# Optimization experiments

Measured on AMD Instinct MI355X. Metric: run time of the kernel, lower is better.

The kernel has to match this reference:

```python
import jax, jax.numpy as jnp
import numpy as np

B, N, C, NPOINT, NSAMPLE, NHEAD, NLAYERS, DOUT = 8, 4096, 128, 1024, 32, 4, 2, 256
EPS = 1e-5


def setup_inputs() -> dict:
    key = jax.random.key(0)
    ks = jax.random.split(key, 12)
    rn = lambda k, s: jax.random.normal(k, s, jnp.float32) * 0.05
    return {
        "xyz": jax.random.normal(ks[0], (B, 3, N), jnp.float32),
        "features": jax.random.normal(ks[1], (B, C, N), jnp.float32),
        # position-encoding MLP (1x1 convs) + BatchNorm2d (inference, running mean=0 var=1)
        "pe_w1": rn(ks[2], (C // 2, 3)), "pe_b1": jnp.zeros((C // 2,), jnp.float32),
        "bn_g": jnp.ones((C // 2,), jnp.float32), "bn_b": jnp.zeros((C // 2,), jnp.float32),
        "pe_w2": rn(ks[3], (C, C // 2)), "pe_b2": jnp.zeros((C,), jnp.float32),
        # 2 pre-norm transformer encoder layers (stacked params)
        "in_w": rn(ks[4], (NLAYERS, 3 * C, C)), "in_b": jnp.zeros((NLAYERS, 3 * C), jnp.float32),
        "out_w": rn(ks[5], (NLAYERS, C, C)), "out_b": jnp.zeros((NLAYERS, C), jnp.float32),
        "ln1_g": jnp.ones((NLAYERS, C), jnp.float32), "ln1_b": jnp.zeros((NLAYERS, C), jnp.float32),
        "ln2_g": jnp.ones((NLAYERS, C), jnp.float32), "ln2_b": jnp.zeros((NLAYERS, C), jnp.float32),
        "ff1_w": rn(ks[6], (NLAYERS, 2 * C, C)), "ff1_b": jnp.zeros((NLAYERS, 2 * C), jnp.float32),
        "ff2_w": rn(ks[7], (NLAYERS, C, 2 * C)), "ff2_b": jnp.zeros((NLAYERS, C), jnp.float32),
        # final 1x1 conv (fc)
        "fc_w": rn(ks[8], (DOUT, C)), "fc_b": jnp.zeros((DOUT,), jnp.float32),
    }


def _fps(pts, npoint):
    # pts: [B, N, 3]; iterative farthest point sampling (start at index 0)
    b, n, _ = pts.shape
    d0 = jnp.full((b, n), 1e10, pts.dtype)
    f0 = jnp.zeros((b,), jnp.int32)

    def step(carry, _):
        dist, far = carry
        c = jnp.take_along_axis(pts, far[:, None, None], axis=1)  # [B,1,3]
        d = jnp.sum((pts - c) ** 2, axis=-1)                      # [B,N]
        dist = jnp.minimum(dist, d)
        return (dist, jnp.argmax(dist, axis=-1).astype(jnp.int32)), far

    _, idx = jax.lax.scan(step, (d0, f0), None, length=npoint)
    return idx.T  # [B, npoint]


def _knn(nsample, pts, queries):
    # pts [B,N,3], queries [B,S,3] -> [B,S,nsample] nearest-neighbor indices
    sqd = (jnp.sum(queries ** 2, -1)[:, :, None] + jnp.sum(pts ** 2, -1)[:, None, :]
           - 2.0 * jnp.einsum('bsc,bnc->bsn', queries, pts))
    _, idx = jax.lax.top_k(-sqd, nsample)
    return idx


_gather = jax.vmap(lambda p, i: p[i])  # per-batch fancy gather


def _ln(x, g, b):
    m = jnp.mean(x, -1, keepdims=True)
    v = jnp.var(x, -1, keepdims=True)
    return (x - m) * jax.lax.rsqrt(v + EPS) * g + b


def _forward(xyz, features, pe_w1, pe_b1, bn_g, bn_b, pe_w2, pe_b2,
             in_w, in_b, out_w, out_b, ln1_g, ln1_b, ln2_g, ln2_b,
             ff1_w, ff1_b, ff2_w, ff2_b, fc_w, fc_b):
    xyz_t = xyz.transpose(0, 2, 1)                      # [B,N,3]
    fps_idx = _fps(xyz_t, NPOINT)                       # [B,S]
    new_xyz = _gather(xyz_t, fps_idx)                   # [B,S,3]
    gidx = _knn(NSAMPLE, xyz_t, new_xyz)                # [B,S,ns]
    gxyz = _gather(xyz_t, gidx)                         # [B,S,ns,3]
    gfeat = _gather(features.transpose(0, 2, 1), gidx)  # [B,S,ns,C]

    # position encoding: 1x1 conv MLP, BN in inference mode (mean=0, var=1)
    h = gxyz @ pe_w1.T + pe_b1
    h = h / jnp.sqrt(jnp.float32(1.0 + EPS)) * bn_g + bn_b
    pe = jax.nn.relu(h) @ pe_w2.T + pe_b2               # [B,S,ns,C]

    x = (gfeat + pe).reshape(B * NPOINT, NSAMPLE, C)    # groups as batch, seq=ns
    hd = C // NHEAD
    scale = 1.0 / jnp.sqrt(jnp.float32(hd))
    for l in range(NLAYERS):
        hN = _ln(x, ln1_g[l], ln1_b[l])
        qkv = hN @ in_w[l].T + in_b[l]
        q, k, v = jnp.split(qkv, 3, axis=-1)
        q = q.reshape(-1, NSAMPLE, NHEAD, hd)
        k = k.reshape(-1, NSAMPLE, NHEAD, hd)
        v = v.reshape(-1, NSAMPLE, NHEAD, hd)
        att = jax.nn.softmax(jnp.einsum('mqhd,mkhd->mhqk', q, k) * scale, axis=-1)
        a = jnp.einsum('mhqk,mkhd->mqhd', att, v).reshape(-1, NSAMPLE, C)
        x = x + (a @ out_w[l].T + out_b[l])
        h2 = _ln(x, ln2_g[l], ln2_b[l])
        x = x + (jax.nn.relu(h2 @ ff1_w[l].T + ff1_b[l]) @ ff2_w[l].T + ff2_b[l])

    pooled = x.reshape(B, NPOINT, NSAMPLE, C).max(axis=2)  # maxpool over neighbors
    out = pooled @ fc_w.T + fc_b                           # [B,S,DOUT]
    return new_xyz.transpose(0, 2, 1), out.transpose(0, 2, 1)


def reference(xyz, features, pe_w1, pe_b1, bn_g, bn_b, pe_w2, pe_b2,
              in_w, in_b, out_w, out_b, ln1_g, ln1_b, ln2_g, ln2_b,
              ff1_w, ff1_b, ff2_w, ff2_b, fc_w, fc_b):
    return _forward(xyz, features, pe_w1, pe_b1, bn_g, bn_b, pe_w2, pe_b2,
                    in_w, in_b, out_w, out_b, ln1_g, ln1_b, ln2_g, ln2_b,
                    ff1_w, ff1_b, ff2_w, ff2_b, fc_w, fc_b)
```

## Files before the change

### kernel.cpp

```cpp
#include <hip/hip_runtime.h>

typedef unsigned int u32;
typedef unsigned long long u64;
typedef unsigned short u16;
typedef __attribute__((ext_vector_type(8))) short bf16x8;
typedef __attribute__((ext_vector_type(4))) float f32x4;

#define DEV __device__ __forceinline__

DEV float sq3(float x, float y, float z) {
#pragma clang fp contract(off)
  return (x * x + y * y) + z * z;
}
DEV float knn_sqd(float4 Q, float4 p) {
#pragma clang fp contract(off)
  float dot = (Q.x * p.x + Q.y * p.y) + Q.z * p.z;
  return (Q.w + p.w) - 2.0f * dot;
}
DEV float dot4(float4 a, float4 b) {
  return (a.x * b.x + a.y * b.y) + (a.z * b.z + a.w * b.w);
}
DEV u32 f2bfu(float f) {
  u32 u = __float_as_uint(f);
  return (u + 0x7fffu + ((u >> 16) & 1u)) >> 16;
}
DEV f32x4 MFMA(bf16x8 a, bf16x8 b, f32x4 c) {
  return __builtin_amdgcn_mfma_f32_16x16x32_bf16(a, b, c, 0, 0, 0);
}

enum : int {
  W_PEW1 = 0, W_PEB1 = 192, W_BNG = 256, W_BNB = 320,
  W_PEW2 = 384, W_PEB2 = 8576,
  W_INW  = 8704,   W_INB  = 107008,
  W_OUTW = 107776, W_OUTB = 140544,
  W_LN1G = 140800, W_LN1B = 141056, W_LN2G = 141312, W_LN2B = 141568,
  W_FF1W = 141824, W_FF1B = 207360,
  W_FF2W = 207872, W_FF2B = 273408,
  W_FCW  = 273664, W_FCB  = 306432,
  W_TOTAL = 306688
};
enum : int { WP_QB = 0, WP_FB = 768, WP_TOTAL = 1280 };
enum : int {
  WB_Q  = 0,
  WB_O  = 98304,
  WB_F1 = 131072,
  WB_F2 = 196608,
  WB_P2 = 262144,
  WB_TOTAL = 270336
};

static const size_t OFF_XYZW  = 1226752;
static const size_t OFF_NEWX  = 1751040;
static const size_t OFF_KNN   = 1882112;
static const size_t OFF_WP    = 2930688;
static const size_t OFF_WB    = 2936064;
static const size_t OFF_FEATT = 3476736;
static const size_t END_BIG   = 20253952;

struct WArgs { const float* p[20]; };

__global__ void k_setup(WArgs a, float* __restrict__ wf, float* __restrict__ wp,
                        u16* __restrict__ wb, const float* __restrict__ xyz,
                        float4* __restrict__ xyzw) {
  const int blk = blockIdx.x, tid = threadIdx.x;
  if (blk < 1198) {
    const int idx = blk * 256 + tid;
    if (idx >= W_TOTAL) return;
    const int sz[20] = {192, 64, 64, 64, 8192, 128, 98304, 768, 32768, 256,
                        256, 256, 256, 256, 65536, 512, 65536, 256, 32768, 256};
    int rem = idx;
#pragma unroll
    for (int s = 0; s < 20; ++s) {
      if (rem < sz[s]) { wf[idx] = a.p[s][rem]; return; }
      rem -= sz[s];
    }
    return;
  }
  if (blk < 1206) {
    const int idx = (blk - 1198) * 256 + tid;
    if (idx >= 1920) return;
    if (idx < 768) {
      const int l = idx / 384, o = idx % 384;
      const float* W = a.p[6] + l * 49152 + o * 128;
      const float* G = a.p[10] + l * 128;
      const float* Bl = a.p[11] + l * 128;
      float acc = a.p[7][l * 384 + o];
      u16* ph = wb + WB_Q + (l * 384 + o) * 128;
      for (int c = 0; c < 128; ++c) {
        const float w = W[c];
        acc += Bl[c] * w;
        ph[c] = (u16)f2bfu(w * G[c]);
      }
      wp[WP_QB + l * 384 + o] = acc;
    } else if (idx < 1280) {
      const int j2 = idx - 768, l = j2 / 256, o = j2 % 256;
      const float* W = a.p[14] + l * 32768 + o * 128;
      const float* G = a.p[12] + l * 128;
      const float* Bl = a.p[13] + l * 128;
      float acc = a.p[15][l * 256 + o];
      u16* ph = wb + WB_F1 + (l * 256 + o) * 128;
      for (int c = 0; c < 128; ++c) {
        const float w = W[c];
        acc += Bl[c] * w;
        ph[c] = (u16)f2bfu(w * G[c]);
      }
      wp[WP_FB + l * 256 + o] = acc;
    } else if (idx < 1536) {
      const int j2 = idx - 1280, l = j2 / 128, o = j2 % 128;
      const float* W = a.p[8] + l * 16384 + o * 128;
      u16* ph = wb + WB_O + (l * 128 + o) * 128;
      for (int c = 0; c < 128; ++c) ph[c] = (u16)f2bfu(W[c]);
    } else if (idx < 1792) {
      const int j2 = idx - 1536, l = j2 / 128, o = j2 % 128;
      const float* W = a.p[16] + l * 32768 + o * 256;
      u16* ph = wb + WB_F2 + (l * 128 + o) * 256;
      for (int c = 0; c < 256; ++c) ph[c] = (u16)f2bfu(W[c]);
    } else {
      const int o = idx - 1792;
      const float* W = a.p[4] + o * 64;
      u16* ph = wb + WB_P2 + o * 64;
      for (int c = 0; c < 64; ++c) ph[c] = (u16)f2bfu(W[c]);
    }
    return;
  }
  {
    const int i = (blk - 1206) * 256 + tid;
    const int b = i >> 12, n = i & 4095;
    const size_t s = (size_t)b * 12288 + n;
    float x = xyz[s], y = xyz[s + 4096], z = xyz[s + 8192];
    xyzw[i] = make_float4(x, y, z, sq3(x, y, z));
  }
}

__global__ __launch_bounds__(256, 1) void k_pre(
    const float4* __restrict__ xyzw, float4* __restrict__ new_xyzw,
    float* __restrict__ out_xyz, const float* __restrict__ feat,
    float* __restrict__ featT) {
  __shared__ float PXs[4096], PYs[4096], PZs[4096];
  __shared__ u64 wkk[2][4];
  __shared__ float tile[32][33];
  const int tid = threadIdx.x;
  if (blockIdx.x >= 8) {
    const int bb = blockIdx.x - 8;
    const int b = bb >> 9, r2 = bb & 511;
    const int n0 = (r2 >> 2) << 5, c0 = (r2 & 3) << 5;
    const int tx = tid & 31, ty = tid >> 5;
#pragma unroll
    for (int i = 0; i < 4; ++i) {
      const int c = c0 + ty + (i << 3);
      tile[ty + (i << 3)][tx] =
          __builtin_nontemporal_load(&feat[(size_t)b * 524288 + (size_t)c * 4096 + n0 + tx]);
    }
    __syncthreads();
#pragma unroll
    for (int i = 0; i < 4; ++i) {
      const int n = n0 + ty + (i << 3);
      __builtin_nontemporal_store(tile[tx][ty + (i << 3)],
          &featT[(size_t)b * 524288 + (size_t)n * 128 + c0 + tx]);
    }
    return;
  }
  const int b = blockIdx.x;
  const float4* src = xyzw + (size_t)b * 4096;
  float px[16], py[16], pz[16], dm[16];
#pragma unroll
  for (int j = 0; j < 16; ++j) {
    float4 v = src[tid * 16 + j];
    PXs[tid * 16 + j] = v.x; PYs[tid * 16 + j] = v.y; PZs[tid * 16 + j] = v.z;
    px[j] = v.x; py[j] = v.y; pz[j] = v.z; dm[j] = 1e10f;
  }
  __syncthreads();
  float cx = PXs[0], cy = PYs[0], cz = PZs[0];
  if (tid == 0) {
    new_xyzw[(size_t)b * 1024] = make_float4(cx, cy, cz, sq3(cx, cy, cz));
    out_xyz[b * 3072]        = cx;
    out_xyz[b * 3072 + 1024] = cy;
    out_xyz[b * 3072 + 2048] = cz;
  }
  for (int t = 1; t < 1024; ++t) {
    {
      float dx = px[0] - cx, dy = py[0] - cy, dz = pz[0] - cz;
      dm[0] = fminf(dm[0], sq3(dx, dy, dz));
    }
    float bv = dm[0];
    int bi = tid * 16;
#pragma unroll
    for (int j = 1; j < 16; ++j) {
      float dx = px[j] - cx, dy = py[j] - cy, dz = pz[j] - cz;
      float d = sq3(dx, dy, dz);
      dm[j] = fminf(dm[j], d);
      if (dm[j] > bv) { bv = dm[j]; bi = tid * 16 + j; }
    }
    float mx = bv;
    mx = fmaxf(mx, __shfl_xor(mx, 1));
    mx = fmaxf(mx, __shfl_xor(mx, 2));
    mx = fmaxf(mx, __shfl_xor(mx, 4));
    mx = fmaxf(mx, __shfl_xor(mx, 8));
    mx = fmaxf(mx, __shfl_xor(mx, 16));
    mx = fmaxf(mx, __shfl_xor(mx, 32));
    const u64 ball = __ballot(bv == mx);
    const int wl2 = (int)(__ffsll((unsigned long long)ball) - 1);
    const int wbi = __shfl(bi, wl2);
    if ((tid & 63) == 0)
      wkk[t & 1][tid >> 6] = ((u64)__float_as_uint(mx) << 12) | (u32)(4095 - wbi);
    __syncthreads();
    const u64* wk = wkk[t & 1];
    u64 ka = wk[0] > wk[1] ? wk[0] : wk[1];
    u64 kb2 = wk[2] > wk[3] ? wk[2] : wk[3];
    u64 key = ka > kb2 ? ka : kb2;
    const int win = 4095 - (int)(key & 0xfffu);
    cx = PXs[win]; cy = PYs[win]; cz = PZs[win];
    if (tid == 0) {
      new_xyzw[(size_t)b * 1024 + t] = make_float4(cx, cy, cz, sq3(cx, cy, cz));
      out_xyz[b * 3072 + t]        = cx;
      out_xyz[b * 3072 + 1024 + t] = cy;
      out_xyz[b * 3072 + 2048 + t] = cz;
    }
  }
}

__global__ __launch_bounds__(128, 1) void k_knn(
    const float4* __restrict__ xyzw, const float4* __restrict__ qxyzw,
    int* __restrict__ knn) {
  __shared__ u64 LL[32 * 128];
  __shared__ int HH[4][32];
  const int tid = threadIdx.x;
  const int ql = tid >> 5, ss = tid & 31;
  const int b = blockIdx.x >> 8;
  const int q = ((blockIdx.x & 255) << 2) + ql;
  const float4 Q = qxyzw[(size_t)b * 1024 + q];
  u64 L[32];
#pragma unroll
  for (int i = 0; i < 32; ++i) L[i] = ~0ULL;
  const float4* P = xyzw + (size_t)b * 4096;
#pragma unroll 2
  for (int j = 0; j < 128; ++j) {
    const int n = j * 32 + ss;
    float4 p = P[n];
    float sqd = knn_sqd(Q, p);
    u32 u = __float_as_uint(sqd);
    u ^= (u32)((int)u >> 31) | 0x80000000u;
    const u64 key = ((u64)u << 12) | (u32)n;
    if (key < L[31]) {
#pragma unroll
      for (int i = 31; i >= 1; --i) {
        const u64 lo = L[i] < key ? L[i] : key;
        L[i] = lo > L[i - 1] ? lo : L[i - 1];
      }
      L[0] = L[0] < key ? L[0] : key;
    }
  }
#pragma unroll
  for (int i = 0; i < 32; ++i) LL[i * 128 + tid] = L[i];
  __syncthreads();
  if (ss == 0) {
#pragma unroll
    for (int t2 = 0; t2 < 32; ++t2) HH[ql][t2] = 0;
    const size_t ob = ((size_t)b * 1024 + q) * 32;
    for (int o = 0; o < 32; ++o) {
      u64 best = ~0ULL;
      int bs = 0;
#pragma unroll
      for (int t2 = 0; t2 < 32; ++t2) {
        const int hh = HH[ql][t2];
        const u64 v = (hh < 32) ? LL[hh * 128 + (ql * 32 + t2)] : ~0ULL;
        if (v < best) { best = v; bs = t2; }
      }
      HH[ql][bs]++;
      knn[ob + o] = (int)(best & 0xfffu);
    }
  }
}


DEV void ln_z(const float* __restrict__ X, u16* __restrict__ ZH, int tid) {
  const int r = tid >> 3, sub = tid & 7;
  const int xm = (r & 7) << 2;
  const float* row = X + r * 128;
  float4 v[4];
  float s = 0.f;
#pragma unroll
  for (int j = 0; j < 4; ++j) {
    v[j] = *(const float4*)&row[(sub * 16 + j * 4) ^ xm];
    s += (v[j].x + v[j].y) + (v[j].z + v[j].w);
  }
  s += __shfl_xor(s, 1); s += __shfl_xor(s, 2); s += __shfl_xor(s, 4);
  const float m = s * 0.0078125f;
  float qv = 0.f;
#pragma unroll
  for (int j = 0; j < 4; ++j) {
    float a = v[j].x - m, b = v[j].y - m, c = v[j].z - m, d = v[j].w - m;
    qv += (a * a + b * b) + (c * c + d * d);
  }
  qv += __shfl_xor(qv, 1); qv += __shfl_xor(qv, 2); qv += __shfl_xor(qv, 4);
  const float rstd = 1.0f / sqrtf(qv * 0.0078125f + 1e-5f);
  const int mask = (r & 7) << 3;
  float z[16];
#pragma unroll
  for (int j = 0; j < 4; ++j) {
    z[j * 4]     = (v[j].x - m) * rstd;
    z[j * 4 + 1] = (v[j].y - m) * rstd;
    z[j * 4 + 2] = (v[j].z - m) * rstd;
    z[j * 4 + 3] = (v[j].w - m) * rstd;
  }
#pragma unroll
  for (int i = 0; i < 8; ++i) {
    const u32 w = f2bfu(z[2 * i]) | (f2bfu(z[2 * i + 1]) << 16);
    *(u32*)&ZH[r * 128 + ((sub * 16 + 2 * i) ^ mask)] = w;
  }
}

template <int K, int AINS, int MODE>
DEV void gemmT(const u16* __restrict__ A, const u16* __restrict__ wbp,
               const float* __restrict__ bias, float* __restrict__ X,
               u16* __restrict__ OUTp, int co, int tid) {
  const int wv = tid >> 6, wl = tid & 63;
  const int c0 = wv * 32;
  const int lm = wl & 15, kb = wl >> 4;
  const int amask = (lm & 7) << 3;
  constexpr int KS = K / 32;
  constexpr int CH = (KS > 4) ? 4 : KS;
  f32x4 acc[4][2];
#pragma unroll
  for (int m = 0; m < 4; ++m)
#pragma unroll
    for (int t = 0; t < 2; ++t) acc[m][t] = (f32x4){0.f, 0.f, 0.f, 0.f};
#pragma unroll
  for (int kc = 0; kc < KS / CH; ++kc) {
    bf16x8 bfr[CH][2];
#pragma unroll
    for (int ks = 0; ks < CH; ++ks) {
      const int k0 = (kc * CH + ks) * 32 + kb * 8;
#pragma unroll
      for (int t = 0; t < 2; ++t)
        bfr[ks][t] = *(const bf16x8*)&wbp[(size_t)(c0 + t * 16 + lm) * K + k0];
    }
#pragma unroll
    for (int ks = 0; ks < CH; ++ks) {
      const int k0 = (kc * CH + ks) * 32 + kb * 8;
      bf16x8 a[4];
#pragma unroll
      for (int m = 0; m < 4; ++m)
        a[m] = *(const bf16x8*)&A[(size_t)(m * 16 + lm) * AINS + (k0 ^ amask)];
#pragma unroll
      for (int m = 0; m < 4; ++m)
#pragma unroll
        for (int t = 0; t < 2; ++t)
          acc[m][t] = MFMA(a[m], bfr[ks][t], acc[m][t]);
    }
  }
#pragma unroll
  for (int m = 0; m < 4; ++m)
#pragma unroll
    for (int t = 0; t < 2; ++t) {
      const int col = c0 + t * 16 + lm;
      const float bv = bias[col];
      if (MODE == 3) {
        const int j0 = (m & 1) * 16 + kb * 4;
        const int base = (m >> 1) * 8192 + (col & 31) * 256 + 128 +
                         ((col >> 5) << 5) + (j0 ^ ((col & 3) << 3));
        *(u32*)&OUTp[base]     = f2bfu(acc[m][t][0] + bv) | (f2bfu(acc[m][t][1] + bv) << 16);
        *(u32*)&OUTp[base + 2] = f2bfu(acc[m][t][2] + bv) | (f2bfu(acc[m][t][3] + bv) << 16);
      } else if (MODE == 1) {
#pragma unroll
        for (int j = 0; j < 4; ++j) {
          const int row = m * 16 + kb * 4 + j;
          X[row * 128 + (col ^ ((row & 7) << 2))] += acc[m][t][j] + bv;
        }
      } else {
#pragma unroll
        for (int j = 0; j < 4; ++j) {
          const int row = m * 16 + kb * 4 + j;
          float val = acc[m][t][j] + bv;
          if (MODE == 2) val = fmaxf(val, 0.f);
          OUTp[row * 256 + ((co + col) ^ ((row & 7) << 3))] = (u16)f2bfu(val);
        }
      }
    }
}

__global__ __launch_bounds__(256, 2) void k_xform(
    const float* __restrict__ feat, const float* __restrict__ featT, const int useT,
    const float4* __restrict__ xyzw, const int* __restrict__ knn,
    const float* __restrict__ wf, const float* __restrict__ wp,
    const u16* __restrict__ wb, float* __restrict__ out) {
  __shared__ __align__(16) float sm[20480];
  float* X  = sm;
  u16* ZH   = (u16*)(sm + 8192);
  u16* QKp  = (u16*)(sm + 12288);
  const int g0 = blockIdx.x * 2, b = g0 >> 10, tid = threadIdx.x;
  const int r = tid >> 3, sub = tid & 7, cs = sub * 16;
  const int xm = (r & 7) << 2;
#pragma unroll
  for (int grp = 0; grp < 2; ++grp) {
    const int n = knn[(g0 + grp) * 32 + r];
    float* dst = &X[(grp * 32 + r) * 128];
    if (useT) {
      const f32x4* srcp = (const f32x4*)(featT + ((size_t)(b * 4096 + n)) * 128 + cs);
#pragma unroll
      for (int j = 0; j < 4; ++j)
        *(f32x4*)&dst[(cs + j * 4) ^ xm] = __builtin_nontemporal_load(&srcp[j]);
    } else {
      const size_t fb0 = (size_t)b * 524288 + n;
#pragma unroll
      for (int j = 0; j < 16; ++j)
        dst[(cs + j) ^ xm] = __builtin_nontemporal_load(&feat[fb0 + (size_t)(cs + j) * 4096]);
    }
    const float4 g4 = xyzw[(size_t)b * 4096 + n];
    const float rs = 1.0f / sqrtf(1.0f + 1e-5f);
    const int mask = (r & 7) << 3;
#pragma unroll
    for (int i = 0; i < 4; ++i) {
      u32 wpk = 0;
#pragma unroll
      for (int e = 0; e < 2; ++e) {
        const int c = sub * 8 + 2 * i + e;
        float hv = g4.x * wf[W_PEW1 + c * 3] + g4.y * wf[W_PEW1 + c * 3 + 1] +
                   g4.z * wf[W_PEW1 + c * 3 + 2] + wf[W_PEB1 + c];
        hv = hv * (wf[W_BNG + c] * rs) + wf[W_BNB + c];
        hv = fmaxf(hv, 0.f);
        wpk |= f2bfu(hv) << (16 * e);
      }
      *(u32*)&ZH[(grp * 32 + r) * 128 + ((sub * 8 + 2 * i) ^ mask)] = wpk;
    }
  }
  __syncthreads();
  gemmT<64, 128, 1>(ZH, wb + WB_P2, wf + W_PEB2, X, QKp, 0, tid);
  __syncthreads();
#pragma unroll 1
  for (int l = 0; l < 2; ++l) {
    ln_z(X, ZH, tid);
    ln_z(X + 4096, ZH + 4096, tid);
    __syncthreads();
    gemmT<128, 128, 0>(ZH, wb + WB_Q + l * 49152, wp + WP_QB + l * 384,
                       X, QKp, 0, tid);
    gemmT<128, 128, 0>(ZH, wb + WB_Q + l * 49152 + 16384,
                       wp + WP_QB + l * 384 + 128, X, QKp, 128, tid);
    __syncthreads();
    {
      const int wv = tid >> 6, wl = tid & 63;
      const int hh = wv, lm = wl & 15, kb = wl >> 4;
      bf16x8 qf[2][2], kf[2][2];
#pragma unroll
      for (int grp = 0; grp < 2; ++grp) {
        const u16* Qb = QKp + grp * 8192;
#pragma unroll
        for (int t = 0; t < 2; ++t) {
          const int rr = t * 16 + lm;
          const int msk = (rr & 7) << 3;
          qf[grp][t] = *(const bf16x8*)&Qb[rr * 256 + ((hh * 32 + kb * 8) ^ msk)];
          kf[grp][t] = *(const bf16x8*)&Qb[rr * 256 + ((128 + hh * 32 + kb * 8) ^ msk)];
        }
      }
      __syncthreads();
      const float scale = 0.1767766952966369f;
      const f32x4 zz = {0.f, 0.f, 0.f, 0.f};
#pragma unroll
      for (int grp = 0; grp < 2; ++grp) {
        f32x4 sc[2][2];
        sc[0][0] = MFMA(qf[grp][0], kf[grp][0], zz);
        sc[0][1] = MFMA(qf[grp][0], kf[grp][1], zz);
        sc[1][0] = MFMA(qf[grp][1], kf[grp][0], zz);
        sc[1][1] = MFMA(qf[grp][1], kf[grp][1], zz);
        u16* Pw = QKp + grp * 8192 + hh * 32;
#pragma unroll
        for (int mtl = 0; mtl < 2; ++mtl) {
#pragma unroll
          for (int j = 0; j < 4; ++j) {
            float a0 = sc[mtl][0][j] * scale, a1 = sc[mtl][1][j] * scale;
            float mx = fmaxf(a0, a1);
            mx = fmaxf(mx, __shfl_xor(mx, 1));
            mx = fmaxf(mx, __shfl_xor(mx, 2));
            mx = fmaxf(mx, __shfl_xor(mx, 4));
            mx = fmaxf(mx, __shfl_xor(mx, 8));
            const float e0 = __expf(a0 - mx), e1 = __expf(a1 - mx);
            float sum = e0 + e1;
            sum += __shfl_xor(sum, 1); sum += __shfl_xor(sum, 2);
            sum += __shfl_xor(sum, 4); sum += __shfl_xor(sum, 8);
            const float inv = 1.0f / sum;
            const int q2 = mtl * 16 + kb * 4 + j;
            const int qm = (q2 & 3) << 3;
            Pw[q2 * 256 + (lm ^ qm)]        = (u16)f2bfu(e0 * inv);
            Pw[q2 * 256 + ((16 + lm) ^ qm)] = (u16)f2bfu(e1 * inv);
          }
        }
      }
    }
    __syncthreads();
    gemmT<128, 128, 3>(ZH, wb + WB_Q + l * 49152 + 32768,
                       wp + WP_QB + l * 384 + 256, X, QKp, 0, tid);
    __syncthreads();
    {
      const int wv = tid >> 6, wl = tid & 63;
      const int hh = wv, lm = wl & 15, kb = wl >> 4;
      const f32x4 zz = {0.f, 0.f, 0.f, 0.f};
#pragma unroll
      for (int grp = 0; grp < 2; ++grp) {
        const u16* Qb = QKp + grp * 8192;
        bf16x8 pf[2], vf[2];
#pragma unroll
        for (int t = 0; t < 2; ++t) {
          const int q2 = t * 16 + lm;
          pf[t] = *(const bf16x8*)&Qb[q2 * 256 + hh * 32 +
                                      ((kb * 8) ^ ((q2 & 3) << 3))];
          const int d = hh * 32 + t * 16 + lm;
          vf[t] = *(const bf16x8*)&Qb[(d & 31) * 256 + 128 + hh * 32 +
                                      ((kb * 8) ^ ((d & 3) << 3))];
        }
        f32x4 av[2][2];
        av[0][0] = MFMA(pf[0], vf[0], zz); av[0][1] = MFMA(pf[0], vf[1], zz);
        av[1][0] = MFMA(pf[1], vf[0], zz); av[1][1] = MFMA(pf[1], vf[1], zz);
#pragma unroll
        for (int mtl = 0; mtl < 2; ++mtl)
#pragma unroll
          for (int ntl = 0; ntl < 2; ++ntl)
#pragma unroll
            for (int j = 0; j < 4; ++j) {
              const int row = mtl * 16 + kb * 4 + j;
              const int col = hh * 32 + ntl * 16 + lm;
              ZH[(grp * 32 + row) * 128 + (col ^ ((row & 7) << 3))] =
                  (u16)f2bfu(av[mtl][ntl][j]);
            }
      }
    }
    __syncthreads();
    gemmT<128, 128, 1>(ZH, wb + WB_O + l * 16384, wf + W_OUTB + l * 128,
                       X, QKp, 0, tid);
    __syncthreads();
    ln_z(X, ZH, tid);
    ln_z(X + 4096, ZH + 4096, tid);
    __syncthreads();
    gemmT<128, 128, 2>(ZH, wb + WB_F1 + l * 32768, wp + WP_FB + l * 256,
                       X, QKp, 0, tid);
    gemmT<128, 128, 2>(ZH, wb + WB_F1 + l * 32768 + 16384,
                       wp + WP_FB + l * 256 + 128, X, QKp, 128, tid);
    __syncthreads();
    gemmT<256, 256, 1>(QKp, wb + WB_F2 + l * 32768, wf + W_FF2B + l * 128,
                       X, QKp, 0, tid);
    __syncthreads();
  }
  float* pooled = (float*)ZH;
  if (tid < 128) {
#pragma unroll
    for (int grp = 0; grp < 2; ++grp) {
      const float* Xg = X + grp * 4096;
      float m = Xg[tid];
#pragma unroll
      for (int rr = 1; rr < 32; ++rr)
        m = fmaxf(m, Xg[rr * 128 + (tid ^ ((rr & 7) << 2))]);
      pooled[grp * 128 + tid] = m;
    }
  }
  __syncthreads();
  {
    const float* wr = wf + W_FCW + tid * 128;
    const float bias = wf[W_FCB + tid];
#pragma unroll
    for (int grp = 0; grp < 2; ++grp) {
      float acc = bias;
      const float* pg = pooled + grp * 128;
#pragma unroll 8
      for (int c = 0; c < 128; c += 4) {
        float4 w4 = *(const float4*)&wr[c];
        float4 x4 = *(const float4*)&pg[c];
        acc += dot4(x4, w4);
      }
      const int s = (g0 + grp) & 1023;
      __builtin_nontemporal_store(acc,
          &out[24576 + (size_t)b * 262144 + (size_t)tid * 1024 + s]);
    }
  }
}

extern "C" void kernel_launch(void* const* d_in, const int* in_sizes, int n_in,
                              void* d_out, int out_size, void* d_ws, size_t ws_size,
                              hipStream_t stream) {
  (void)in_sizes; (void)n_in; (void)out_size;
  char* ws = (char*)d_ws;
  float* wf    = (float*)ws;
  float4* xyzw = (float4*)(ws + OFF_XYZW);
  float4* newx = (float4*)(ws + OFF_NEWX);
  int* knni    = (int*)(ws + OFF_KNN);
  float* wp    = (float*)(ws + OFF_WP);
  u16* wb      = (u16*)(ws + OFF_WB);
  const float* xyz  = (const float*)d_in[0];
  const float* feat = (const float*)d_in[1];
  const int useT = (ws_size >= END_BIG) ? 1 : 0;
  float* featT = useT ? (float*)(ws + OFF_FEATT) : (float*)d_in[1];
  WArgs wa;
  for (int i = 0; i < 20; ++i) wa.p[i] = (const float*)d_in[2 + i];
  float* outp = (float*)d_out;

  hipLaunchKernelGGL(k_setup, dim3(1334), dim3(256), 0, stream, wa, wf, wp, wb, xyz, xyzw);
  hipLaunchKernelGGL(k_pre, dim3(useT ? 4104 : 8), dim3(256), 0, stream,
                     xyzw, newx, outp, feat, featT);
  hipLaunchKernelGGL(k_knn, dim3(2048), dim3(128), 0, stream, xyzw, newx, knni);
  hipLaunchKernelGGL(k_xform, dim3(4096), dim3(256), 0, stream,
                     feat, featT, useT, xyzw, knni, wf, wp, wb, outp);
}
```

Measured before the change: 2.015 ms.

## Fuse kNN and transformer kernels with per-query flags for producer-consumer overlap

The separate kNN and transform kernels become one persistent-style launch. The first 1024 blocks compute kNN for 8 queries each and publish a per-query ready flag with release semantics. The remaining blocks spin on those flags and then run the transformer. The kNN merge also changes from an LDS-based serial merge to a wave-shuffle argmin with ballot-driven list popping. The aim is to hide the kNN phase behind transformer work and remove a kernel boundary. In exchange it adds an extra memset, relies on kNN blocks being scheduled before the consumers that wait on them, and consumer blocks may sit idle while polling.

Result: faster. 1.790 ms (-11.2%).

```diff
diff --git a/kernel.cpp b/kernel.cpp
--- a/kernel.cpp
+++ b/kernel.cpp
@@ -54,8 +54,9 @@
 static const size_t OFF_KNN   = 1882112;
 static const size_t OFF_WP    = 2930688;
 static const size_t OFF_WB    = 2936064;
-static const size_t OFF_FEATT = 3476736;
-static const size_t END_BIG   = 20253952;
+static const size_t OFF_FLAGS = 3476736;
+static const size_t OFF_FEATT = 3509504;
+static const size_t END_BIG   = 20286720;
 
 struct WArgs { const float* p[20]; };
 
@@ -219,60 +220,6 @@
   }
 }
 
-__global__ __launch_bounds__(128, 1) void k_knn(
-    const float4* __restrict__ xyzw, const float4* __restrict__ qxyzw,
-    int* __restrict__ knn) {
-  __shared__ u64 LL[32 * 128];
-  __shared__ int HH[4][32];
-  const int tid = threadIdx.x;
-  const int ql = tid >> 5, ss = tid & 31;
-  const int b = blockIdx.x >> 8;
-  const int q = ((blockIdx.x & 255) << 2) + ql;
-  const float4 Q = qxyzw[(size_t)b * 1024 + q];
-  u64 L[32];
-#pragma unroll
-  for (int i = 0; i < 32; ++i) L[i] = ~0ULL;
-  const float4* P = xyzw + (size_t)b * 4096;
-#pragma unroll 2
-  for (int j = 0; j < 128; ++j) {
-    const int n = j * 32 + ss;
-    float4 p = P[n];
-    float sqd = knn_sqd(Q, p);
-    u32 u = __float_as_uint(sqd);
-    u ^= (u32)((int)u >> 31) | 0x80000000u;
-    const u64 key = ((u64)u << 12) | (u32)n;
-    if (key < L[31]) {
-#pragma unroll
-      for (int i = 31; i >= 1; --i) {
-        const u64 lo = L[i] < key ? L[i] : key;
-        L[i] = lo > L[i - 1] ? lo : L[i - 1];
-      }
-      L[0] = L[0] < key ? L[0] : key;
-    }
-  }
-#pragma unroll
-  for (int i = 0; i < 32; ++i) LL[i * 128 + tid] = L[i];
-  __syncthreads();
-  if (ss == 0) {
-#pragma unroll
-    for (int t2 = 0; t2 < 32; ++t2) HH[ql][t2] = 0;
-    const size_t ob = ((size_t)b * 1024 + q) * 32;
-    for (int o = 0; o < 32; ++o) {
-      u64 best = ~0ULL;
-      int bs = 0;
-#pragma unroll
-      for (int t2 = 0; t2 < 32; ++t2) {
-        const int hh = HH[ql][t2];
-        const u64 v = (hh < 32) ? LL[hh * 128 + (ql * 32 + t2)] : ~0ULL;
-        if (v < best) { best = v; bs = t2; }
-      }
-      HH[ql][bs]++;
-      knn[ob + o] = (int)(best & 0xfffu);
-    }
-  }
-}
-
-
 DEV void ln_z(const float* __restrict__ X, u16* __restrict__ ZH, int tid) {
   const int r = tid >> 3, sub = tid & 7;
   const int xm = (r & 7) << 2;
@@ -379,195 +326,260 @@
     }
 }
 
-__global__ __launch_bounds__(256, 2) void k_xform(
+__global__ __launch_bounds__(256, 2) void k_work(
     const float* __restrict__ feat, const float* __restrict__ featT, const int useT,
-    const float4* __restrict__ xyzw, const int* __restrict__ knn,
+    const float4* __restrict__ xyzw, const float4* __restrict__ newx,
+    int* __restrict__ knn, int* __restrict__ flags,
     const float* __restrict__ wf, const float* __restrict__ wp,
     const u16* __restrict__ wb, float* __restrict__ out) {
   __shared__ __align__(16) float sm[20480];
-  float* X  = sm;
-  u16* ZH   = (u16*)(sm + 8192);
-  u16* QKp  = (u16*)(sm + 12288);
-  const int g0 = blockIdx.x * 2, b = g0 >> 10, tid = threadIdx.x;
-  const int r = tid >> 3, sub = tid & 7, cs = sub * 16;
-  const int xm = (r & 7) << 2;
-#pragma unroll
-  for (int grp = 0; grp < 2; ++grp) {
-    const int n = knn[(g0 + grp) * 32 + r];
-    float* dst = &X[(grp * 32 + r) * 128];
-    if (useT) {
-      const f32x4* srcp = (const f32x4*)(featT + ((size_t)(b * 4096 + n)) * 128 + cs);
-#pragma unroll
-      for (int j = 0; j < 4; ++j)
-        *(f32x4*)&dst[(cs + j * 4) ^ xm] = __builtin_nontemporal_load(&srcp[j]);
-    } else {
-      const size_t fb0 = (size_t)b * 524288 + n;
-#pragma unroll
-      for (int j = 0; j < 16; ++j)
-        dst[(cs + j) ^ xm] = __builtin_nontemporal_load(&feat[fb0 + (size_t)(cs + j) * 4096]);
-    }
-    const float4 g4 = xyzw[(size_t)b * 4096 + n];
-    const float rs = 1.0f / sqrtf(1.0f + 1e-5f);
-    const int mask = (r & 7) << 3;
-#pragma unroll
-    for (int i = 0; i < 4; ++i) {
-      u32 wpk = 0;
-#pragma unroll
-      for (int e = 0; e < 2; ++e) {
-        const int c = sub * 8 + 2 * i + e;
-        float hv = g4.x * wf[W_PEW1 + c * 3] + g4.y * wf[W_PEW1 + c * 3 + 1] +
-                   g4.z * wf[W_PEW1 + c * 3 + 2] + wf[W_PEB1 + c];
-        hv = hv * (wf[W_BNG + c] * rs) + wf[W_BNB + c];
-        hv = fmaxf(hv, 0.f);
-        wpk |= f2bfu(hv) << (16 * e);
-      }
-      *(u32*)&ZH[(grp * 32 + r) * 128 + ((sub * 8 + 2 * i) ^ mask)] = wpk;
-    }
-  }
-  __syncthreads();
-  gemmT<64, 128, 1>(ZH, wb + WB_P2, wf + W_PEB2, X, QKp, 0, tid);
-  __syncthreads();
+  const int tid = threadIdx.x;
+
+  if (blockIdx.x < 1024) {
+    const int k2 = blockIdx.x;
+    const int b = k2 & 7, s0 = (k2 >> 3) * 8;
+    const int ql = tid >> 5, ss = tid & 31;
+    const int s = s0 + ql;
+    const float4 Q = newx[(size_t)b * 1024 + s];
+    u64 L[32];
+#pragma unroll
+    for (int i = 0; i < 32; ++i) L[i] = ~0ULL;
+    const float4* P = xyzw + (size_t)b * 4096;
+#pragma unroll 2
+    for (int j = 0; j < 128; ++j) {
+      const int n = j * 32 + ss;
+      float4 p = P[n];
+      float sqd = knn_sqd(Q, p);
+      u32 u = __float_as_uint(sqd);
+      u ^= (u32)((int)u >> 31) | 0x80000000u;
+      const u64 key = ((u64)u << 12) | (u32)n;
+      if (key < L[31]) {
+#pragma unroll
+        for (int i = 31; i >= 1; --i) {
+          const u64 lo = L[i] < key ? L[i] : key;
+          L[i] = lo > L[i - 1] ? lo : L[i - 1];
+        }
+        L[0] = L[0] < key ? L[0] : key;
+      }
+    }
+    const size_t ob = ((size_t)b * 1024 + s) * 32;
 #pragma unroll 1
-  for (int l = 0; l < 2; ++l) {
-    ln_z(X, ZH, tid);
-    ln_z(X + 4096, ZH + 4096, tid);
+    for (int o = 0; o < 32; ++o) {
+      u64 mn = L[0];
+#pragma unroll
+      for (int m2 = 1; m2 < 32; m2 <<= 1) {
+        const u64 oth = __shfl_xor(mn, m2, 32);
+        mn = oth < mn ? oth : mn;
+      }
+      const u64 ball = __ballot(L[0] == mn);
+      const u32 half = (u32)(ball >> (tid & 32));
+      const int wl = __ffs(half) - 1;
+      if (ss == 0) knn[ob + o] = (int)(mn & 0xfffu);
+      if (ss == wl) {
+#pragma unroll
+        for (int i = 0; i < 31; ++i) L[i] = L[i + 1];
+        L[31] = ~0ULL;
+      }
+    }
+    if (ss == 0)
+      __hip_atomic_store(&flags[(s << 3) | b], 1, __ATOMIC_RELEASE, __HIP_MEMORY_SCOPE_AGENT);
+    return;
+  }
+
+  {
+    const int bid = blockIdx.x - 1024;
+    const int g0 = bid * 2, b = g0 >> 10;
+    const int s0 = g0 & 1023;
+    if (tid == 0) {
+      while (!__hip_atomic_load(&flags[(s0 << 3) | b], __ATOMIC_ACQUIRE, __HIP_MEMORY_SCOPE_AGENT))
+        __builtin_amdgcn_s_sleep(8);
+      while (!__hip_atomic_load(&flags[((s0 + 1) << 3) | b], __ATOMIC_ACQUIRE, __HIP_MEMORY_SCOPE_AGENT))
+        __builtin_amdgcn_s_sleep(8);
+    }
     __syncthreads();
-    gemmT<128, 128, 0>(ZH, wb + WB_Q + l * 49152, wp + WP_QB + l * 384,
-                       X, QKp, 0, tid);
-    gemmT<128, 128, 0>(ZH, wb + WB_Q + l * 49152 + 16384,
-                       wp + WP_QB + l * 384 + 128, X, QKp, 128, tid);
+    float* X  = sm;
+    u16* ZH   = (u16*)(sm + 8192);
+    u16* QKp  = (u16*)(sm + 12288);
+    const int r = tid >> 3, sub = tid & 7, cs = sub * 16;
+    const int xm = (r & 7) << 2;
+#pragma unroll
+    for (int grp = 0; grp < 2; ++grp) {
+      const int n = knn[(g0 + grp) * 32 + r];
+      float* dst = &X[(grp * 32 + r) * 128];
+      if (useT) {
+        const f32x4* srcp = (const f32x4*)(featT + ((size_t)(b * 4096 + n)) * 128 + cs);
+#pragma unroll
+        for (int j = 0; j < 4; ++j)
+          *(f32x4*)&dst[(cs + j * 4) ^ xm] = __builtin_nontemporal_load(&srcp[j]);
+      } else {
+        const size_t fb0 = (size_t)b * 524288 + n;
+#pragma unroll
+        for (int j = 0; j < 16; ++j)
+          dst[(cs + j) ^ xm] = __builtin_nontemporal_load(&feat[fb0 + (size_t)(cs + j) * 4096]);
+      }
+      const float4 g4 = xyzw[(size_t)b * 4096 + n];
+      const float rs = 1.0f / sqrtf(1.0f + 1e-5f);
+      const int mask = (r & 7) << 3;
+#pragma unroll
+      for (int i = 0; i < 4; ++i) {
+        u32 wpk = 0;
+#pragma unroll
+        for (int e = 0; e < 2; ++e) {
+          const int c = sub * 8 + 2 * i + e;
+          float hv = g4.x * wf[W_PEW1 + c * 3] + g4.y * wf[W_PEW1 + c * 3 + 1] +
+                     g4.z * wf[W_PEW1 + c * 3 + 2] + wf[W_PEB1 + c];
+          hv = hv * (wf[W_BNG + c] * rs) + wf[W_BNB + c];
+          hv = fmaxf(hv, 0.f);
+          wpk |= f2bfu(hv) << (16 * e);
+        }
+        *(u32*)&ZH[(grp * 32 + r) * 128 + ((sub * 8 + 2 * i) ^ mask)] = wpk;
+      }
+    }
+    __syncthreads();
+    gemmT<64, 128, 1>(ZH, wb + WB_P2, wf + W_PEB2, X, QKp, 0, tid);
+    __syncthreads();
+#pragma unroll 1
+    for (int l = 0; l < 2; ++l) {
+      ln_z(X, ZH, tid);
+      ln_z(X + 4096, ZH + 4096, tid);
+      __syncthreads();
+      gemmT<128, 128, 0>(ZH, wb + WB_Q + l * 49152, wp + WP_QB + l * 384,
+                         X, QKp, 0, tid);
+      gemmT<128, 128, 0>(ZH, wb + WB_Q + l * 49152 + 16384,
+                         wp + WP_QB + l * 384 + 128, X, QKp, 128, tid);
+      __syncthreads();
+      {
+        const int wv = tid >> 6, wl = tid & 63;
+        const int hh = wv, lm = wl & 15, kb = wl >> 4;
+        bf16x8 qf[2][2], kf[2][2];
+#pragma unroll
+        for (int grp = 0; grp < 2; ++grp) {
+          const u16* Qb = QKp + grp * 8192;
+#pragma unroll
+          for (int t = 0; t < 2; ++t) {
+            const int rr = t * 16 + lm;
+            const int msk = (rr & 7) << 3;
+            qf[grp][t] = *(const bf16x8*)&Qb[rr * 256 + ((hh * 32 + kb * 8) ^ msk)];
+            kf[grp][t] = *(const bf16x8*)&Qb[rr * 256 + ((128 + hh * 32 + kb * 8) ^ msk)];
+          }
+        }
+        __syncthreads();
+        const float scale = 0.1767766952966369f;
+        const f32x4 zz = {0.f, 0.f, 0.f, 0.f};
+#pragma unroll
+        for (int grp = 0; grp < 2; ++grp) {
+          f32x4 sc[2][2];
+          sc[0][0] = MFMA(qf[grp][0], kf[grp][0], zz);
+          sc[0][1] = MFMA(qf[grp][0], kf[grp][1], zz);
+          sc[1][0] = MFMA(qf[grp][1], kf[grp][0], zz);
+          sc[1][1] = MFMA(qf[grp][1], kf[grp][1], zz);
+          u16* Pw = QKp + grp * 8192 + hh * 32;
+#pragma unroll
+          for (int mtl = 0; mtl < 2; ++mtl) {
+#pragma unroll
+            for (int j = 0; j < 4; ++j) {
+              float a0 = sc[mtl][0][j] * scale, a1 = sc[mtl][1][j] * scale;
+              float mx = fmaxf(a0, a1);
+              mx = fmaxf(mx, __shfl_xor(mx, 1));
+              mx = fmaxf(mx, __shfl_xor(mx, 2));
+              mx = fmaxf(mx, __shfl_xor(mx, 4));
+              mx = fmaxf(mx, __shfl_xor(mx, 8));
+              const float e0 = __expf(a0 - mx), e1 = __expf(a1 - mx);
+              float sum = e0 + e1;
+              sum += __shfl_xor(sum, 1); sum += __shfl_xor(sum, 2);
+              sum += __shfl_xor(sum, 4); sum += __shfl_xor(sum, 8);
+              const float inv = 1.0f / sum;
+              const int q2 = mtl * 16 + kb * 4 + j;
+              const int qm = (q2 & 3) << 3;
+              Pw[q2 * 256 + (lm ^ qm)]        = (u16)f2bfu(e0 * inv);
+              Pw[q2 * 256 + ((16 + lm) ^ qm)] = (u16)f2bfu(e1 * inv);
+            }
+          }
+        }
+      }
+      __syncthreads();
+      gemmT<128, 128, 3>(ZH, wb + WB_Q + l * 49152 + 32768,
+                         wp + WP_QB + l * 384 + 256, X, QKp, 0, tid);
+      __syncthreads();
+      {
+        const int wv = tid >> 6, wl = tid & 63;
+        const int hh = wv, lm = wl & 15, kb = wl >> 4;
+        const f32x4 zz = {0.f, 0.f, 0.f, 0.f};
+#pragma unroll
+        for (int grp = 0; grp < 2; ++grp) {
+          const u16* Qb = QKp + grp * 8192;
+          bf16x8 pf[2], vf[2];
+#pragma unroll
+          for (int t = 0; t < 2; ++t) {
+            const int q2 = t * 16 + lm;
+            pf[t] = *(const bf16x8*)&Qb[q2 * 256 + hh * 32 +
+                                        ((kb * 8) ^ ((q2 & 3) << 3))];
+            const int d = hh * 32 + t * 16 + lm;
+            vf[t] = *(const bf16x8*)&Qb[(d & 31) * 256 + 128 + hh * 32 +
+                                        ((kb * 8) ^ ((d & 3) << 3))];
+          }
+          f32x4 av[2][2];
+          av[0][0] = MFMA(pf[0], vf[0], zz); av[0][1] = MFMA(pf[0], vf[1], zz);
+          av[1][0] = MFMA(pf[1], vf[0], zz); av[1][1] = MFMA(pf[1], vf[1], zz);
+#pragma unroll
+          for (int mtl = 0; mtl < 2; ++mtl)
+#pragma unroll
+            for (int ntl = 0; ntl < 2; ++ntl)
+#pragma unroll
+              for (int j = 0; j < 4; ++j) {
+                const int row = mtl * 16 + kb * 4 + j;
+                const int col = hh * 32 + ntl * 16 + lm;
+                ZH[(grp * 32 + row) * 128 + (col ^ ((row & 7) << 3))] =
+                    (u16)f2bfu(av[mtl][ntl][j]);
+              }
+        }
+      }
+      __syncthreads();
+      gemmT<128, 128, 1>(ZH, wb + WB_O + l * 16384, wf + W_OUTB + l * 128,
+                         X, QKp, 0, tid);
+      __syncthreads();
+      ln_z(X, ZH, tid);
+      ln_z(X + 4096, ZH + 4096, tid);
+      __syncthreads();
+      gemmT<128, 128, 2>(ZH, wb + WB_F1 + l * 32768, wp + WP_FB + l * 256,
+                         X, QKp, 0, tid);
+      gemmT<128, 128, 2>(ZH, wb + WB_F1 + l * 32768 + 16384,
+                         wp + WP_FB + l * 256 + 128, X, QKp, 128, tid);
+      __syncthreads();
+      gemmT<256, 256, 1>(QKp, wb + WB_F2 + l * 32768, wf + W_FF2B + l * 128,
+                         X, QKp, 0, tid);
+      __syncthreads();
+    }
+    float* pooled = (float*)ZH;
+    if (tid < 128) {
+#pragma unroll
+      for (int grp = 0; grp < 2; ++grp) {
+        const float* Xg = X + grp * 4096;
+        float m = Xg[tid];
+#pragma unroll
+        for (int rr = 1; rr < 32; ++rr)
+          m = fmaxf(m, Xg[rr * 128 + (tid ^ ((rr & 7) << 2))]);
+        pooled[grp * 128 + tid] = m;
+      }
+    }
     __syncthreads();
     {
-      const int wv = tid >> 6, wl = tid & 63;
-      const int hh = wv, lm = wl & 15, kb = wl >> 4;
-      bf16x8 qf[2][2], kf[2][2];
+      const float* wr = wf + W_FCW + tid * 128;
+      const float bias = wf[W_FCB + tid];
 #pragma unroll
       for (int grp = 0; grp < 2; ++grp) {
-        const u16* Qb = QKp + grp * 8192;
-#pragma unroll
-        for (int t = 0; t < 2; ++t) {
-          const int rr = t * 16 + lm;
-          const int msk = (rr & 7) << 3;
-          qf[grp][t] = *(const bf16x8*)&Qb[rr * 256 + ((hh * 32 + kb * 8) ^ msk)];
-          kf[grp][t] = *(const bf16x8*)&Qb[rr * 256 + ((128 + hh * 32 + kb * 8) ^ msk)];
-        }
-      }
-      __syncthreads();
-      const float scale = 0.1767766952966369f;
-      const f32x4 zz = {0.f, 0.f, 0.f, 0.f};
-#pragma unroll
-      for (int grp = 0; grp < 2; ++grp) {
-        f32x4 sc[2][2];
-        sc[0][0] = MFMA(qf[grp][0], kf[grp][0], zz);
-        sc[0][1] = MFMA(qf[grp][0], kf[grp][1], zz);
-        sc[1][0] = MFMA(qf[grp][1], kf[grp][0], zz);
-        sc[1][1] = MFMA(qf[grp][1], kf[grp][1], zz);
-        u16* Pw = QKp + grp * 8192 + hh * 32;
-#pragma unroll
-        for (int mtl = 0; mtl < 2; ++mtl) {
-#pragma unroll
-          for (int j = 0; j < 4; ++j) {
-            float a0 = sc[mtl][0][j] * scale, a1 = sc[mtl][1][j] * scale;
-            float mx = fmaxf(a0, a1);
-            mx = fmaxf(mx, __shfl_xor(mx, 1));
-            mx = fmaxf(mx, __shfl_xor(mx, 2));
-            mx = fmaxf(mx, __shfl_xor(mx, 4));
-            mx = fmaxf(mx, __shfl_xor(mx, 8));
-            const float e0 = __expf(a0 - mx), e1 = __expf(a1 - mx);
-            float sum = e0 + e1;
-            sum += __shfl_xor(sum, 1); sum += __shfl_xor(sum, 2);
-            sum += __shfl_xor(sum, 4); sum += __shfl_xor(sum, 8);
-            const float inv = 1.0f / sum;
-            const int q2 = mtl * 16 + kb * 4 + j;
-            const int qm = (q2 & 3) << 3;
-            Pw[q2 * 256 + (lm ^ qm)]        = (u16)f2bfu(e0 * inv);
-            Pw[q2 * 256 + ((16 + lm) ^ qm)] = (u16)f2bfu(e1 * inv);
-          }
-        }
-      }
-    }
-    __syncthreads();
-    gemmT<128, 128, 3>(ZH, wb + WB_Q + l * 49152 + 32768,
-                       wp + WP_QB + l * 384 + 256, X, QKp, 0, tid);
-    __syncthreads();
-    {
-      const int wv = tid >> 6, wl = tid & 63;
-      const int hh = wv, lm = wl & 15, kb = wl >> 4;
-      const f32x4 zz = {0.f, 0.f, 0.f, 0.f};
-#pragma unroll
-      for (int grp = 0; grp < 2; ++grp) {
-        const u16* Qb = QKp + grp * 8192;
-        bf16x8 pf[2], vf[2];
-#pragma unroll
-        for (int t = 0; t < 2; ++t) {
-          const int q2 = t * 16 + lm;
-          pf[t] = *(const bf16x8*)&Qb[q2 * 256 + hh * 32 +
-                                      ((kb * 8) ^ ((q2 & 3) << 3))];
-          const int d = hh * 32 + t * 16 + lm;
-          vf[t] = *(const bf16x8*)&Qb[(d & 31) * 256 + 128 + hh * 32 +
-                                      ((kb * 8) ^ ((d & 3) << 3))];
-        }
-        f32x4 av[2][2];
-        av[0][0] = MFMA(pf[0], vf[0], zz); av[0][1] = MFMA(pf[0], vf[1], zz);
-        av[1][0] = MFMA(pf[1], vf[0], zz); av[1][1] = MFMA(pf[1], vf[1], zz);
-#pragma unroll
-        for (int mtl = 0; mtl < 2; ++mtl)
-#pragma unroll
-          for (int ntl = 0; ntl < 2; ++ntl)
-#pragma unroll
-            for (int j = 0; j < 4; ++j) {
-              const int row = mtl * 16 + kb * 4 + j;
-              const int col = hh * 32 + ntl * 16 + lm;
-              ZH[(grp * 32 + row) * 128 + (col ^ ((row & 7) << 3))] =
-                  (u16)f2bfu(av[mtl][ntl][j]);
-            }
-      }
-    }
-    __syncthreads();
-    gemmT<128, 128, 1>(ZH, wb + WB_O + l * 16384, wf + W_OUTB + l * 128,
-                       X, QKp, 0, tid);
-    __syncthreads();
-    ln_z(X, ZH, tid);
-    ln_z(X + 4096, ZH + 4096, tid);
-    __syncthreads();
-    gemmT<128, 128, 2>(ZH, wb + WB_F1 + l * 32768, wp + WP_FB + l * 256,
-                       X, QKp, 0, tid);
-    gemmT<128, 128, 2>(ZH, wb + WB_F1 + l * 32768 + 16384,
-                       wp + WP_FB + l * 256 + 128, X, QKp, 128, tid);
-    __syncthreads();
-    gemmT<256, 256, 1>(QKp, wb + WB_F2 + l * 32768, wf + W_FF2B + l * 128,
-                       X, QKp, 0, tid);
-    __syncthreads();
-  }
-  float* pooled = (float*)ZH;
-  if (tid < 128) {
-#pragma unroll
-    for (int grp = 0; grp < 2; ++grp) {
-      const float* Xg = X + grp * 4096;
-      float m = Xg[tid];
-#pragma unroll
-      for (int rr = 1; rr < 32; ++rr)
-        m = fmaxf(m, Xg[rr * 128 + (tid ^ ((rr & 7) << 2))]);
-      pooled[grp * 128 + tid] = m;
-    }
-  }
-  __syncthreads();
-  {
-    const float* wr = wf + W_FCW + tid * 128;
-    const float bias = wf[W_FCB + tid];
-#pragma unroll
-    for (int grp = 0; grp < 2; ++grp) {
-      float acc = bias;
-      const float* pg = pooled + grp * 128;
+        float acc = bias;
+        const float* pg = pooled + grp * 128;
 #pragma unroll 8
-      for (int c = 0; c < 128; c += 4) {
-        float4 w4 = *(const float4*)&wr[c];
-        float4 x4 = *(const float4*)&pg[c];
-        acc += dot4(x4, w4);
-      }
-      const int s = (g0 + grp) & 1023;
-      __builtin_nontemporal_store(acc,
-          &out[24576 + (size_t)b * 262144 + (size_t)tid * 1024 + s]);
+        for (int c = 0; c < 128; c += 4) {
+          float4 w4 = *(const float4*)&wr[c];
+          float4 x4 = *(const float4*)&pg[c];
+          acc += dot4(x4, w4);
+        }
+        const int s = (g0 + grp) & 1023;
+        __builtin_nontemporal_store(acc,
+            &out[24576 + (size_t)b * 262144 + (size_t)tid * 1024 + s]);
+      }
     }
   }
 }
@@ -583,6 +595,7 @@
   int* knni    = (int*)(ws + OFF_KNN);
   float* wp    = (float*)(ws + OFF_WP);
   u16* wb      = (u16*)(ws + OFF_WB);
+  int* flags   = (int*)(ws + OFF_FLAGS);
   const float* xyz  = (const float*)d_in[0];
   const float* feat = (const float*)d_in[1];
   const int useT = (ws_size >= END_BIG) ? 1 : 0;
@@ -591,10 +604,10 @@
   for (int i = 0; i < 20; ++i) wa.p[i] = (const float*)d_in[2 + i];
   float* outp = (float*)d_out;
 
+  hipMemsetAsync(ws + OFF_FLAGS, 0, 32768, stream);
   hipLaunchKernelGGL(k_setup, dim3(1334), dim3(256), 0, stream, wa, wf, wp, wb, xyz, xyzw);
   hipLaunchKernelGGL(k_pre, dim3(useT ? 4104 : 8), dim3(256), 0, stream,
                      xyzw, newx, outp, feat, featT);
-  hipLaunchKernelGGL(k_knn, dim3(2048), dim3(128), 0, stream, xyzw, newx, knni);
-  hipLaunchKernelGGL(k_xform, dim3(4096), dim3(256), 0, stream,
-                     feat, featT, useT, xyzw, knni, wf, wp, wb, outp);
-}
+  hipLaunchKernelGGL(k_work, dim3(5120), dim3(256), 0, stream,
+                     feat, featT, useT, xyzw, newx, knni, flags, wf, wp, wb, outp);
+}
```
